# Optimization experiments

Measured on AMD Instinct MI355X. Metric: run time of the kernel, lower is better.

## Reference

```python
import jax, jax.numpy as jnp
import numpy as np

B, S, D, H = 4, 2048, 1024, 16
HD = D // H  # head dim = 64

def setup_inputs() -> dict:
    key = jax.random.key(0)
    ks = jax.random.split(key, 11)
    s = 1.0 / np.sqrt(D)
    return {
        "q": jax.random.normal(ks[0], (B, S, D), jnp.float32),
        "k": jax.random.normal(ks[1], (B, S, D), jnp.float32),
        "v": jax.random.normal(ks[2], (B, S, D), jnp.float32),
        "Wq": jax.random.normal(ks[3], (D, D), jnp.float32) * s,
        "bq": jnp.zeros((D,), jnp.float32),
        "Wk": jax.random.normal(ks[4], (D, D), jnp.float32) * s,
        "bk": jnp.zeros((D,), jnp.float32),
        "Wv": jax.random.normal(ks[5], (D, D), jnp.float32) * s,
        "bv": jnp.zeros((D,), jnp.float32),
        "Wo": jax.random.normal(ks[6], (D, D), jnp.float32) * s,
        "bo": jnp.zeros((D,), jnp.float32),
    }

def reference(q, k, v, Wq, bq, Wk, bk, Wv, bv, Wo, bo):
    b, n, _ = q.shape
    # QKV projections, split heads -> [b, s, h, hd]
    qh = (q @ Wq + bq).reshape(b, n, H, HD)
    kh = (k @ Wk + bk).reshape(b, k.shape[1], H, HD)
    vh = (v @ Wv + bv).reshape(b, v.shape[1], H, HD)
    scale = 1.0 / np.sqrt(HD)
    scores = jnp.einsum('blhe,bshe->bhls', qh, kh)  # [b,h,l,s]
    attn = jax.nn.softmax(scale * scores, axis=-1)  # dropout is identity in eval
    out = jnp.einsum('bhls,bshd->blhd', attn, vh)   # [b,l,h,hd]
    out = out.reshape(b, n, H * HD)
    return out @ Wo + bo
```

## Files before the change

kernel.cpp:

```cpp
#include <hip/hip_runtime.h>
#include <cstdint>

#define DEV __device__ __forceinline__

typedef __attribute__((ext_vector_type(8))) __bf16 bf16x8;
typedef __attribute__((ext_vector_type(2))) unsigned u32x2;
typedef __attribute__((ext_vector_type(4))) float f32x4;

DEV unsigned short f2b(float f) {
  unsigned u = __builtin_bit_cast(unsigned, f);
  u += 0x7fffu + ((u >> 16) & 1u);
  return (unsigned short)(u >> 16);
}

DEV unsigned pkrn(float f0, float f1) {
  unsigned a0 = __builtin_bit_cast(unsigned, f0) + 0x8000u;
  unsigned a1 = __builtin_bit_cast(unsigned, f1) + 0x8000u;
#if __has_builtin(__builtin_amdgcn_perm)
  return __builtin_amdgcn_perm(a1, a0, 0x07060302u);
#else
  return (a0 >> 16) | (a1 & 0xffff0000u);
#endif
}

DEV float exp2_fast(float x) {
#if __has_builtin(__builtin_amdgcn_exp2f)
  return __builtin_amdgcn_exp2f(x);
#else
  return __expf(x * 0.6931471805599453f);
#endif
}

DEV void gload_lds16(const unsigned short* g, unsigned short* l) {
  __builtin_amdgcn_global_load_lds(
      (const __attribute__((address_space(1))) void*)g,
      (__attribute__((address_space(3))) void*)l, 16, 0, 0);
}

__global__ __launch_bounds__(256) void cvt3_kernel(const float* __restrict__ q,
                                                   const float* __restrict__ k,
                                                   const float* __restrict__ v,
                                                   unsigned short* __restrict__ dst) {
  int z = blockIdx.y;
  const float* src = (z == 0) ? q : (z == 1) ? k : v;
  unsigned short* d = dst + (size_t)z * 8192 * 1024;
  int i = blockIdx.x * 256 + threadIdx.x;
  const float4* s4 = (const float4*)src;
  float4 a = s4[2 * i], b = s4[2 * i + 1];
  uint4 o;
  o.x = (unsigned)f2b(a.x) | ((unsigned)f2b(a.y) << 16);
  o.y = (unsigned)f2b(a.z) | ((unsigned)f2b(a.w) << 16);
  o.z = (unsigned)f2b(b.x) | ((unsigned)f2b(b.y) << 16);
  o.w = (unsigned)f2b(b.z) | ((unsigned)f2b(b.w) << 16);
  ((uint4*)d)[i] = o;
}

__global__ __launch_bounds__(256) void wtr4_kernel(const float* __restrict__ W0,
                                                   const float* __restrict__ W1,
                                                   const float* __restrict__ W2,
                                                   const float* __restrict__ W3,
                                                   unsigned short* __restrict__ WtBase) {
  int z = blockIdx.z;
  const float* W = (z == 0) ? W0 : (z == 1) ? W1 : (z == 2) ? W2 : W3;
  unsigned short* Wt = WtBase + (size_t)z * 1024 * 1024;
  __shared__ float t[64][65];
  int n0 = blockIdx.x * 64, k0 = blockIdx.y * 64;
  int tx = threadIdx.x & 63, ty = threadIdx.x >> 6;
  for (int i = ty; i < 64; i += 4)
    t[i][tx] = W[(size_t)(k0 + i) * 1024 + n0 + tx];
  __syncthreads();
  for (int i = ty; i < 64; i += 4)
    Wt[(size_t)(n0 + i) * 1024 + k0 + tx] = f2b(t[tx][i]);
}

struct GemmAcc {
  f32x4 acc[4][4];
};

DEV void gemm_core(const unsigned short* __restrict__ A,
                   const unsigned short* __restrict__ Bt,
                   unsigned short* Al, unsigned short* Bl,
                   int m0, int n0, int K, GemmAcc& R) {
  int tid = threadIdx.x, wv = tid >> 6, ln = tid & 63;
  int wr = wv >> 1, wc = wv & 1;
  for (int i = 0; i < 4; i++)
    for (int j = 0; j < 4; j++) R.acc[i][j] = (f32x4)0.f;
  int lr = ln >> 3, lc = (ln & 7) * 8;
  for (int kt = 0; kt < K; kt += 64) {
    __syncthreads();
    for (int o = 0; o < 4; ++o) {
      int op = wv * 4 + o;
      int row = op * 8 + lr;
      gload_lds16(A + (size_t)(m0 + row) * K + kt + lc, &Al[op * 512]);
    }
    for (int o = 0; o < 4; ++o) {
      int op = wv * 4 + o;
      int row = op * 8 + lr;
      gload_lds16(Bt + (size_t)(n0 + row) * K + kt + lc, &Bl[op * 512]);
    }
    __syncthreads();
    for (int kk = 0; kk < 2; ++kk) {
      bf16x8 af[4], bfr[4];
      int ko = kk * 32 + (ln >> 4) * 8;
      for (int i = 0; i < 4; ++i)
        af[i] = *(const bf16x8*)&Al[(wr * 64 + i * 16 + (ln & 15)) * 64 + ko];
      for (int j = 0; j < 4; ++j)
        bfr[j] = *(const bf16x8*)&Bl[(wc * 64 + j * 16 + (ln & 15)) * 64 + ko];
      for (int i = 0; i < 4; ++i)
        for (int j = 0; j < 4; ++j)
          R.acc[i][j] = __builtin_amdgcn_mfma_f32_16x16x32_bf16(af[i], bfr[j], R.acc[i][j], 0, 0, 0);
    }
  }
}

__global__ __launch_bounds__(256) void gemm_qkv(const unsigned short* __restrict__ Xbase,
                                                const unsigned short* __restrict__ Wbase,
                                                const float* __restrict__ bq,
                                                const float* __restrict__ bk,
                                                const float* __restrict__ bv,
                                                unsigned short* __restrict__ Obase,
                                                float qscale) {
  __shared__ unsigned short Al[128 * 64];
  __shared__ unsigned short Bl[128 * 64];
  int z = blockIdx.z;
  const size_t NX = (size_t)8192 * 1024, NW = (size_t)1024 * 1024;
  const unsigned short* A = Xbase + (size_t)z * NX;
  const unsigned short* Bt = Wbase + (size_t)z * NW;
  const float* bias = (z == 0) ? bq : (z == 1) ? bk : bv;
  unsigned short* outp = Obase + (size_t)z * NX;
  int m0 = blockIdx.x * 128, n0 = blockIdx.y * 128;
  GemmAcc R;
  gemm_core(A, Bt, Al, Bl, m0, n0, 1024, R);
  int ln = threadIdx.x & 63, wv = threadIdx.x >> 6;
  int wr = wv >> 1, wc = wv & 1;
  int g = ln >> 4, c = ln & 15;
  if (z < 2) {
    float oscale = (z == 0) ? qscale : 1.0f;
    for (int j = 0; j < 4; ++j) {
      int gn = n0 + wc * 64 + j * 16 + c;
      float bs = bias[gn];
      int h_ = gn >> 6, hd = gn & 63;
      for (int i = 0; i < 4; ++i) {
        int gm0 = m0 + wr * 64 + i * 16 + g * 4;
        for (int r = 0; r < 4; ++r) {
          float vv = (R.acc[i][j][r] + bs) * oscale;
          int gm = gm0 + r;
          int b_ = gm >> 11, s_ = gm & 2047;
          outp[(((size_t)(b_ * 16 + h_) * 2048 + s_) << 6) + hd] = f2b(vv);
        }
      }
    }
  } else {
    int mb = m0 + wr * 64;
    int b_ = mb >> 11, st = (mb & 2047) >> 6;
    for (int j = 0; j < 4; ++j) {
      int gn = n0 + wc * 64 + j * 16 + c;
      float bs = bias[gn];
      int h_ = gn >> 6, hd = gn & 63;
      unsigned short* vrow = outp + (((size_t)((b_ * 16 + h_) * 32 + st) * 64 + hd) << 6);
      for (int r = 0; r < 4; ++r) {
        u32x2 w;
        w.x = pkrn(R.acc[0][j][r] + bs, R.acc[1][j][r] + bs);
        w.y = pkrn(R.acc[2][j][r] + bs, R.acc[3][j][r] + bs);
        *(u32x2*)&vrow[(g * 4 + r) * 4] = w;
      }
    }
  }
}

__global__ __launch_bounds__(256) void gemm_out(const unsigned short* __restrict__ A,
                                                const unsigned short* __restrict__ Bt,
                                                const float* __restrict__ bias,
                                                float* __restrict__ outp) {
  __shared__ unsigned short Al[128 * 64];
  __shared__ unsigned short Bl[128 * 64];
  int m0 = blockIdx.x * 128, n0 = blockIdx.y * 128;
  GemmAcc R;
  gemm_core(A, Bt, Al, Bl, m0, n0, 1024, R);
  int ln = threadIdx.x & 63, wv = threadIdx.x >> 6;
  int wr = wv >> 1, wc = wv & 1;
  int g = ln >> 4, c = ln & 15;
  for (int j = 0; j < 4; ++j) {
    int gn = n0 + wc * 64 + j * 16 + c;
    float bs = bias[gn];
    for (int i = 0; i < 4; ++i) {
      int gm0 = m0 + wr * 64 + i * 16 + g * 4;
      for (int r = 0; r < 4; ++r)
        outp[(size_t)(gm0 + r) * 1024 + gn] = R.acc[i][j][r] + bs;
    }
  }
}

__global__ __launch_bounds__(512, 4) void attn_kernel(const unsigned short* __restrict__ Qh,
                                                      const unsigned short* __restrict__ Kh,
                                                      const unsigned short* __restrict__ VtG,
                                                      unsigned short* __restrict__ AttnOut) {
  __shared__ unsigned short Kl[2][64 * 64];
  __shared__ unsigned short Vl[2][64 * 64];
  __shared__ unsigned short Pl[8 * 32 * 72];
  int tid = threadIdx.x, wv = tid >> 6, ln = tid & 63;
  int qt = blockIdx.x, bh = blockIdx.y;
  const unsigned short* Qb = Qh + (size_t)bh * 2048 * 64;
  const unsigned short* Kb = Kh + (size_t)bh * 2048 * 64;
  const unsigned short* Vb = VtG + (size_t)bh * 2048 * 64;
  int q0 = qt * 256 + wv * 32;
  int g = ln >> 4, c = ln & 15;
  int lr = ln >> 3, lb = ln & 7;
  int rb = wv * 8;
  bf16x8 aq[2][2];
  for (int mi = 0; mi < 2; ++mi)
    for (int kk = 0; kk < 2; ++kk)
      aq[mi][kk] = *(const bf16x8*)(Qb + (size_t)(q0 + mi * 16 + c) * 64 + kk * 32 + g * 8);
  f32x4 o[2][4], lrun[2];
  for (int mi = 0; mi < 2; ++mi) {
    lrun[mi] = (f32x4)0.f;
    for (int j = 0; j < 4; ++j) o[mi][j] = (f32x4)0.f;
  }
  unsigned short* pw = &Pl[wv * 32 * 72];
  gload_lds16(Kb + (size_t)(rb + lr) * 64 + (lb ^ lr) * 8, &Kl[0][rb * 64]);
  gload_lds16(Vb + (size_t)(rb + lr) * 64 + (lb ^ lr) * 8, &Vl[0][rb * 64]);
  __syncthreads();
  for (int t = 0; t < 32; ++t) {
    int cur = t & 1;
    if (t < 31) {
      gload_lds16(Kb + (size_t)((t + 1) * 64 + rb + lr) * 64 + (lb ^ lr) * 8, &Kl[cur ^ 1][rb * 64]);
      const unsigned short* vtb = Vb + (size_t)(t + 1) * 4096;
      gload_lds16(vtb + (size_t)(rb + lr) * 64 + (lb ^ lr) * 8, &Vl[cur ^ 1][rb * 64]);
    }
    f32x4 s[2][4];
    {
      bf16x8 bk0[4], bk1[4];
      for (int j = 0; j < 4; ++j)
        bk0[j] = *(const bf16x8*)&Kl[cur][(j * 16 + c) * 64 + (g ^ (c & 7)) * 8];
      for (int mi = 0; mi < 2; ++mi)
        for (int j = 0; j < 4; ++j)
          s[mi][j] = __builtin_amdgcn_mfma_f32_16x16x32_bf16(aq[mi][0], bk0[j], (f32x4)0.f, 0, 0, 0);
      for (int j = 0; j < 4; ++j)
        bk1[j] = *(const bf16x8*)&Kl[cur][(j * 16 + c) * 64 + ((4 + g) ^ (c & 7)) * 8];
      for (int mi = 0; mi < 2; ++mi)
        for (int j = 0; j < 4; ++j)
          s[mi][j] = __builtin_amdgcn_mfma_f32_16x16x32_bf16(aq[mi][1], bk1[j], s[mi][j], 0, 0, 0);
    }
    for (int mi = 0; mi < 2; ++mi)
      for (int j = 0; j < 4; ++j)
        for (int r = 0; r < 4; ++r) {
          float p = exp2_fast(s[mi][j][r]);
          s[mi][j][r] = p;
          lrun[mi][r] += p;
        }
    for (int mi = 0; mi < 2; ++mi)
      for (int r = 0; r < 4; ++r) {
        u32x2 w;
        w.x = pkrn(s[mi][0][r], s[mi][1][r]);
        w.y = pkrn(s[mi][2][r], s[mi][3][r]);
        *(u32x2*)&pw[(mi * 16 + g * 4 + r) * 72 + c * 4] = w;
      }
    __threadfence_block();
    for (int kk = 0; kk < 2; ++kk) {
      int ko = kk * 32 + g * 8;
      bf16x8 ap[2], bv[4];
      for (int mi = 0; mi < 2; ++mi) ap[mi] = *(const bf16x8*)&pw[(mi * 16 + c) * 72 + ko];
      for (int j = 0; j < 4; ++j)
        bv[j] = *(const bf16x8*)&Vl[cur][(j * 16 + c) * 64 + ((kk * 4 + g) ^ (c & 7)) * 8];
      for (int mi = 0; mi < 2; ++mi)
        for (int j = 0; j < 4; ++j)
          o[mi][j] = __builtin_amdgcn_mfma_f32_16x16x32_bf16(ap[mi], bv[j], o[mi][j], 0, 0, 0);
    }
    __syncthreads();
  }
  int b_ = bh >> 4, h_ = bh & 15;
  for (int mi = 0; mi < 2; ++mi) {
    float linv[4];
    for (int r = 0; r < 4; ++r) {
      float l = lrun[mi][r];
      for (int d = 1; d < 16; d <<= 1) l += __shfl_xor(l, d);
      linv[r] = 1.f / l;
    }
    for (int j = 0; j < 4; ++j)
      for (int r = 0; r < 4; ++r) {
        int row = q0 + mi * 16 + g * 4 + r;
        int col = h_ * 64 + j * 16 + c;
        float val = o[mi][j][r] * linv[r];
        AttnOut[((size_t)b_ * 2048 + row) * 1024 + col] = f2b(val);
      }
  }
}

extern "C" void kernel_launch(void* const* d_in, const int* in_sizes, int n_in,
                              void* d_out, int out_size, void* d_ws, size_t ws_size,
                              hipStream_t stream) {
  const float* q  = (const float*)d_in[0];
  const float* k  = (const float*)d_in[1];
  const float* v  = (const float*)d_in[2];
  const float* Wq = (const float*)d_in[3];
  const float* bq = (const float*)d_in[4];
  const float* Wk = (const float*)d_in[5];
  const float* bk = (const float*)d_in[6];
  const float* Wv = (const float*)d_in[7];
  const float* bv = (const float*)d_in[8];
  const float* Wo = (const float*)d_in[9];
  const float* bo = (const float*)d_in[10];
  float* out = (float*)d_out;

  unsigned short* ws = (unsigned short*)d_ws;
  const size_t NX = (size_t)8192 * 1024;
  const size_t NW = (size_t)1024 * 1024;
  unsigned short* X   = ws;
  unsigned short* Wt  = X + 3 * NX;
  unsigned short* QKV = Wt + 4 * NW;
  unsigned short* Ao  = X;

  const float qscale = 0.125f * 1.4426950408889634f;

  cvt3_kernel<<<dim3(4096, 3), 256, 0, stream>>>(q, k, v, X);
  wtr4_kernel<<<dim3(16, 16, 4), 256, 0, stream>>>(Wq, Wk, Wv, Wo, Wt);
  gemm_qkv<<<dim3(64, 8, 3), 256, 0, stream>>>(X, Wt, bq, bk, bv, QKV, qscale);
  attn_kernel<<<dim3(8, 64), 512, 0, stream>>>(QKV, QKV + NX, QKV + 2 * NX, Ao);
  gemm_out<<<dim3(64, 8), 256, 0, stream>>>(Ao, Wt + 3 * NW, bo, out);
}
```

Before: 361.0 us.

## Keep attention probabilities in registers by computing transposed scores, dropping LDS P buffer

```diff
diff --git a/kernel.cpp b/kernel.cpp
--- a/kernel.cpp
+++ b/kernel.cpp
@@ -5,6 +5,7 @@
 
 typedef __attribute__((ext_vector_type(8))) __bf16 bf16x8;
 typedef __attribute__((ext_vector_type(2))) unsigned u32x2;
+typedef __attribute__((ext_vector_type(4))) unsigned u32x4;
 typedef __attribute__((ext_vector_type(4))) float f32x4;
 
 DEV unsigned short f2b(float f) {
@@ -21,6 +22,15 @@
 #else
   return (a0 >> 16) | (a1 & 0xffff0000u);
 #endif
+}
+
+DEV bf16x8 pack8(const f32x4 a, const f32x4 b) {
+  u32x4 u;
+  u.x = pkrn(a[0], a[1]);
+  u.y = pkrn(a[2], a[3]);
+  u.z = pkrn(b[0], b[1]);
+  u.w = pkrn(b[2], b[3]);
+  return __builtin_bit_cast(bf16x8, u);
 }
 
 DEV float exp2_fast(float x) {
@@ -158,11 +168,11 @@
       float bs = bias[gn];
       int h_ = gn >> 6, hd = gn & 63;
       unsigned short* vrow = outp + (((size_t)((b_ * 16 + h_) * 32 + st) * 64 + hd) << 6);
-      for (int r = 0; r < 4; ++r) {
+      for (int i = 0; i < 4; ++i) {
         u32x2 w;
-        w.x = pkrn(R.acc[0][j][r] + bs, R.acc[1][j][r] + bs);
-        w.y = pkrn(R.acc[2][j][r] + bs, R.acc[3][j][r] + bs);
-        *(u32x2*)&vrow[(g * 4 + r) * 4] = w;
+        w.x = pkrn(R.acc[i][j][0] + bs, R.acc[i][j][1] + bs);
+        w.y = pkrn(R.acc[i][j][2] + bs, R.acc[i][j][3] + bs);
+        *(u32x2*)&vrow[(i & 1) * 32 + g * 8 + (i >> 1) * 4] = w;
       }
     }
   }
@@ -191,13 +201,12 @@
   }
 }
 
-__global__ __launch_bounds__(512, 4) void attn_kernel(const unsigned short* __restrict__ Qh,
+__global__ __launch_bounds__(512, 6) void attn_kernel(const unsigned short* __restrict__ Qh,
                                                       const unsigned short* __restrict__ Kh,
                                                       const unsigned short* __restrict__ VtG,
                                                       unsigned short* __restrict__ AttnOut) {
   __shared__ unsigned short Kl[2][64 * 64];
   __shared__ unsigned short Vl[2][64 * 64];
-  __shared__ unsigned short Pl[8 * 32 * 72];
   int tid = threadIdx.x, wv = tid >> 6, ln = tid & 63;
   int qt = blockIdx.x, bh = blockIdx.y;
   const unsigned short* Qb = Qh + (size_t)bh * 2048 * 64;
@@ -211,12 +220,10 @@
   for (int mi = 0; mi < 2; ++mi)
     for (int kk = 0; kk < 2; ++kk)
       aq[mi][kk] = *(const bf16x8*)(Qb + (size_t)(q0 + mi * 16 + c) * 64 + kk * 32 + g * 8);
-  f32x4 o[2][4], lrun[2];
-  for (int mi = 0; mi < 2; ++mi) {
-    lrun[mi] = (f32x4)0.f;
+  f32x4 o[2][4];
+  float lsum[2] = {0.f, 0.f};
+  for (int mi = 0; mi < 2; ++mi)
     for (int j = 0; j < 4; ++j) o[mi][j] = (f32x4)0.f;
-  }
-  unsigned short* pw = &Pl[wv * 32 * 72];
   gload_lds16(Kb + (size_t)(rb + lr) * 64 + (lb ^ lr) * 8, &Kl[0][rb * 64]);
   gload_lds16(Vb + (size_t)(rb + lr) * 64 + (lb ^ lr) * 8, &Vl[0][rb * 64]);
   __syncthreads();
@@ -227,62 +234,56 @@
       const unsigned short* vtb = Vb + (size_t)(t + 1) * 4096;
       gload_lds16(vtb + (size_t)(rb + lr) * 64 + (lb ^ lr) * 8, &Vl[cur ^ 1][rb * 64]);
     }
-    f32x4 s[2][4];
+    f32x4 ps[4][2];
     {
       bf16x8 bk0[4], bk1[4];
-      for (int j = 0; j < 4; ++j)
-        bk0[j] = *(const bf16x8*)&Kl[cur][(j * 16 + c) * 64 + (g ^ (c & 7)) * 8];
+      for (int jb = 0; jb < 4; ++jb)
+        bk0[jb] = *(const bf16x8*)&Kl[cur][(jb * 16 + c) * 64 + (g ^ (c & 7)) * 8];
+      for (int jb = 0; jb < 4; ++jb)
+        for (int mi = 0; mi < 2; ++mi)
+          ps[jb][mi] = __builtin_amdgcn_mfma_f32_16x16x32_bf16(bk0[jb], aq[mi][0], (f32x4)0.f, 0, 0, 0);
+      for (int jb = 0; jb < 4; ++jb)
+        bk1[jb] = *(const bf16x8*)&Kl[cur][(jb * 16 + c) * 64 + ((4 + g) ^ (c & 7)) * 8];
+      for (int jb = 0; jb < 4; ++jb)
+        for (int mi = 0; mi < 2; ++mi)
+          ps[jb][mi] = __builtin_amdgcn_mfma_f32_16x16x32_bf16(bk1[jb], aq[mi][1], ps[jb][mi], 0, 0, 0);
+    }
+    for (int jb = 0; jb < 4; ++jb)
       for (int mi = 0; mi < 2; ++mi)
-        for (int j = 0; j < 4; ++j)
-          s[mi][j] = __builtin_amdgcn_mfma_f32_16x16x32_bf16(aq[mi][0], bk0[j], (f32x4)0.f, 0, 0, 0);
-      for (int j = 0; j < 4; ++j)
-        bk1[j] = *(const bf16x8*)&Kl[cur][(j * 16 + c) * 64 + ((4 + g) ^ (c & 7)) * 8];
-      for (int mi = 0; mi < 2; ++mi)
-        for (int j = 0; j < 4; ++j)
-          s[mi][j] = __builtin_amdgcn_mfma_f32_16x16x32_bf16(aq[mi][1], bk1[j], s[mi][j], 0, 0, 0);
-    }
-    for (int mi = 0; mi < 2; ++mi)
-      for (int j = 0; j < 4; ++j)
         for (int r = 0; r < 4; ++r) {
-          float p = exp2_fast(s[mi][j][r]);
-          s[mi][j][r] = p;
-          lrun[mi][r] += p;
+          float p = exp2_fast(ps[jb][mi][r]);
+          ps[jb][mi][r] = p;
+          lsum[mi] += p;
         }
-    for (int mi = 0; mi < 2; ++mi)
-      for (int r = 0; r < 4; ++r) {
-        u32x2 w;
-        w.x = pkrn(s[mi][0][r], s[mi][1][r]);
-        w.y = pkrn(s[mi][2][r], s[mi][3][r]);
-        *(u32x2*)&pw[(mi * 16 + g * 4 + r) * 72 + c * 4] = w;
-      }
-    __threadfence_block();
+    bf16x8 ap[2][2];
+    for (int mi = 0; mi < 2; ++mi) {
+      ap[mi][0] = pack8(ps[0][mi], ps[2][mi]);
+      ap[mi][1] = pack8(ps[1][mi], ps[3][mi]);
+    }
     for (int kk = 0; kk < 2; ++kk) {
-      int ko = kk * 32 + g * 8;
-      bf16x8 ap[2], bv[4];
-      for (int mi = 0; mi < 2; ++mi) ap[mi] = *(const bf16x8*)&pw[(mi * 16 + c) * 72 + ko];
+      bf16x8 bv[4];
       for (int j = 0; j < 4; ++j)
         bv[j] = *(const bf16x8*)&Vl[cur][(j * 16 + c) * 64 + ((kk * 4 + g) ^ (c & 7)) * 8];
       for (int mi = 0; mi < 2; ++mi)
         for (int j = 0; j < 4; ++j)
-          o[mi][j] = __builtin_amdgcn_mfma_f32_16x16x32_bf16(ap[mi], bv[j], o[mi][j], 0, 0, 0);
+          o[mi][j] = __builtin_amdgcn_mfma_f32_16x16x32_bf16(ap[mi][kk], bv[j], o[mi][j], 0, 0, 0);
     }
     __syncthreads();
   }
   int b_ = bh >> 4, h_ = bh & 15;
   for (int mi = 0; mi < 2; ++mi) {
-    float linv[4];
+    float l = lsum[mi];
+    l += __shfl_xor(l, 16);
+    l += __shfl_xor(l, 32);
+    float linv_own = 1.f / l;
     for (int r = 0; r < 4; ++r) {
-      float l = lrun[mi][r];
-      for (int d = 1; d < 16; d <<= 1) l += __shfl_xor(l, d);
-      linv[r] = 1.f / l;
-    }
-    for (int j = 0; j < 4; ++j)
-      for (int r = 0; r < 4; ++r) {
-        int row = q0 + mi * 16 + g * 4 + r;
+      float li = __shfl(linv_own, g * 4 + r);
+      int row = q0 + mi * 16 + g * 4 + r;
+      for (int j = 0; j < 4; ++j) {
         int col = h_ * 64 + j * 16 + c;
-        float val = o[mi][j][r] * linv[r];
-        AttnOut[((size_t)b_ * 2048 + row) * 1024 + col] = f2b(val);
+        AttnOut[((size_t)b_ * 2048 + row) * 1024 + col] = f2b(o[mi][j][r] * li);
       }
+    }
   }
 }
 
```

New measurement: 687.5 us. +90.4%, slower.
